# Optimization experiments

Measured on AMD Instinct MI355X. Metric: run time of the kernel, lower is better.

## Reference

```python
import jax, jax.numpy as jnp
import numpy as np

NUM_HEAD = 8
ATTN_DIM = 512
WINDOW_WIDTH = 31
HALF_WIN = WINDOW_WIDTH // 2  # symmetric band half-width
NEG_INF = -1e10


def setup_inputs() -> dict:
    key = jax.random.key(0)
    k0, k1, k2 = jax.random.split(key, 3)
    n, c, w = 4, 512, 2048
    out_dim = 512
    input_ = jax.random.normal(k0, (n, c, 1, w), dtype=jnp.float32)
    mask = jnp.ones((n, w), dtype=jnp.float32)  # 1 = valid key position
    # xavier-uniform-like init for the two linears, zero bias (as in the module)
    lim_in = np.sqrt(6.0 / (c + 3 * ATTN_DIM)).astype(np.float32)
    W_in = jax.random.uniform(k1, (3 * ATTN_DIM, c), jnp.float32, -lim_in, lim_in)
    b_in = jnp.zeros((3 * ATTN_DIM,), jnp.float32)
    lim_fc = np.sqrt(6.0 / (ATTN_DIM + out_dim)).astype(np.float32)
    W_fc = jax.random.uniform(k2, (out_dim, ATTN_DIM), jnp.float32, -lim_fc, lim_fc)
    b_fc = jnp.zeros((out_dim,), jnp.float32)
    return {"input_": input_, "mask": mask, "W_in": W_in, "b_in": b_in,
            "W_fc": W_fc, "b_fc": b_fc}


def reference(input_, mask, W_in, b_in, W_fc, b_fc):
    n, c, h, w = input_.shape  # h == 1
    d = ATTN_DIM // NUM_HEAD
    x = input_.reshape(n, c, w).transpose(0, 2, 1)          # [n, w, c]
    temp = x @ W_in.T + b_in                                # [n, w, 3A]
    temp = temp.transpose(0, 2, 1)                          # [n, 3A, w]
    # channel layout after chunk(num_head) then chunk(3): [h, {q,k,v}, d]
    qkv = temp.reshape(n, NUM_HEAD, 3, d, w)
    q, k, v = qkv[:, :, 0], qkv[:, :, 1], qkv[:, :, 2]      # each [n, H, d, w]
    scale = NUM_HEAD / ATTN_DIM                              # == 1/d_head
    attn = jnp.einsum('nhdi,nhdj->nhij', q, k) * scale       # [n, H, w, w]
    # windowed band mask combined with per-key padding mask (clip_mask/mha_mask)
    idx = jnp.arange(w)
    band = jnp.abs(idx[:, None] - idx[None, :]) <= HALF_WIN  # [w, w]
    valid = band[None, None, :, :] & (mask > 0.5)[:, None, None, :]
    attn = jnp.where(valid, attn, NEG_INF)                   # pre-softmax mask
    attn = jax.nn.softmax(attn, axis=-1)
    attn = jnp.where(valid, attn, 0.0)                       # post-softmax mask
    # dropout in eval mode (identity) for a deterministic reference
    out = jnp.einsum('nhdj,nhij->nhdi', v, attn)             # [n, H, d, w]
    out = out.reshape(n, ATTN_DIM, w).transpose(0, 2, 1)     # [n, w, A]
    out = out @ W_fc.T + b_fc                                # [n, w, out_dim]
    od = out.shape[-1]
    return out.transpose(0, 2, 1).reshape(n, od, 1, w)
```

## Files before the change

kernel.cpp:

```cpp
#include <hip/hip_runtime.h>
#include <hip/hip_bf16.h>
#include <math.h>

#define W_SEQ   2048
#define C_IN    512
#define N_BATCH 4
#define NHEAD   8
#define QKV_CH  1536
#define OUT_CH  512
#define ATTND   512
#define N1_4    (QKV_CH * C_IN / 4)
#define N2_4    (OUT_CH * ATTND / 4)

typedef __attribute__((ext_vector_type(8))) short bf16x8;
typedef __attribute__((ext_vector_type(8))) unsigned short u16x8;
typedef __attribute__((ext_vector_type(4))) float f32x4;

__device__ __forceinline__ void gld16(const void* g, void* l) {
    __builtin_amdgcn_global_load_lds((const __attribute__((address_space(1))) void*)g,
                                     (__attribute__((address_space(3))) void*)l, 16, 0, 0);
}
__device__ __forceinline__ unsigned short f2bf(float f) {
    unsigned u = __float_as_uint(f);
    return (unsigned short)((u + 0x7FFFu + ((u >> 16) & 1u)) >> 16);
}
__device__ __forceinline__ unsigned ld_flag(const unsigned* p) {
    return __hip_atomic_load(p, __ATOMIC_RELAXED, __HIP_MEMORY_SCOPE_AGENT);
}


__device__ __forceinline__ void prep_unit(char* sm, int b,
    const float* __restrict__ input, unsigned short* __restrict__ Xh,
    const float* __restrict__ W_in, unsigned short* __restrict__ Winh,
    const float* __restrict__ W_fc, unsigned short* __restrict__ Wfch)
{
    const int t = threadIdx.x;
    float (*ts)[65] = (float(*)[65])sm;
    const int n  = b >> 8, rm = b & 255;
    const int i0 = (rm & 31) * 64, c0 = (rm >> 5) * 64;
    const int tx = t & 63, ty = t >> 6;
    #pragma unroll
    for (int s = 0; s < 16; ++s) {
        const int c = s * 4 + ty;
        ts[c][tx] = input[((size_t)(n * C_IN + c0 + c)) * W_SEQ + i0 + tx];
    }
    __syncthreads();
    const int c8 = t & 7, il = t >> 3;
    #pragma unroll
    for (int s = 0; s < 2; ++s) {
        const int i = il + 32 * s;
        u16x8 hv;
        #pragma unroll
        for (int e = 0; e < 8; ++e) hv[e] = f2bf(ts[c8 * 8 + e][i]);
        *(u16x8*)(&Xh[((size_t)(n * W_SEQ + i0 + i)) * C_IN + c0 + c8 * 8]) = hv;
    }
    const int idx = b * 256 + t;
    if (idx < N1_4) {
        const float4 v = ((const float4*)W_in)[idx];
        ushort4 hh; hh.x = f2bf(v.x); hh.y = f2bf(v.y); hh.z = f2bf(v.z); hh.w = f2bf(v.w);
        ((ushort4*)Winh)[idx] = hh;
    } else {
        const int j = idx - N1_4;
        const float4 v = ((const float4*)W_fc)[j];
        ushort4 hh; hh.x = f2bf(v.x); hh.y = f2bf(v.y); hh.z = f2bf(v.z); hh.w = f2bf(v.w);
        ((ushort4*)Wfch)[j] = hh;
    }
}

template<int EPI>
__device__ __forceinline__ void gemm_body(char* sm, int bx, int by,
    const unsigned short* __restrict__ A, const unsigned short* __restrict__ B,
    const float* __restrict__ bias, void* __restrict__ Cv, const int ldc)
{
    const int t = threadIdx.x;
    const int l = t & 63, w = t >> 6;
    const int m0 = by * 128, n0 = bx * 128;
    const int wm = w >> 1, wn = w & 1;

    const int subrow = l >> 3;
    const int swz    = ((l & 7) ^ subrow) << 4;
    const char* pA = (const char*)A + (size_t)m0 * 1024 + swz;
    const char* pB = (const char*)B + (size_t)n0 * 1024 + swz;

    const int frow = l & 15;
    f32x4 acc[4][4] = {};

    for (int k0 = 0; k0 < 512; k0 += 64) {
        const int kb = k0 * 2;
        #pragma unroll
        for (int c = 0; c < 4; ++c) {
            const int q = 4 * w + c;
            const size_t roff = (size_t)(q * 8 + subrow) * 1024 + kb;
            gld16(pA + roff, sm +         q * 1024);
            gld16(pB + roff, sm + 16384 + q * 1024);
        }
        __syncthreads();
        #pragma unroll
        for (int kk = 0; kk < 2; ++kk) {
            const int cswz = (kk * 64 + ((l >> 4) << 4)) ^ ((l & 7) << 4);
            bf16x8 a[4], b[4];
            #pragma unroll
            for (int mi = 0; mi < 4; ++mi)
                a[mi] = *(const bf16x8*)(sm + (wm * 64 + mi * 16 + frow) * 128 + cswz);
            #pragma unroll
            for (int ni = 0; ni < 4; ++ni)
                b[ni] = *(const bf16x8*)(sm + 16384 + (wn * 64 + ni * 16 + frow) * 128 + cswz);
            #pragma unroll
            for (int mi = 0; mi < 4; ++mi)
                #pragma unroll
                for (int ni = 0; ni < 4; ++ni)
                    acc[mi][ni] = __builtin_amdgcn_mfma_f32_16x16x32_bf16(a[mi], b[ni], acc[mi][ni], 0, 0, 0);
        }
        __syncthreads();
    }

    const int g = l >> 4;
    int cols[4]; float bcol[4];
    #pragma unroll
    for (int ni = 0; ni < 4; ++ni) {
        cols[ni] = n0 + wn * 64 + ni * 16 + frow;
        bcol[ni] = (EPI == 0) ? bias[cols[ni]] : 0.f;
    }
    #pragma unroll
    for (int mi = 0; mi < 4; ++mi) {
        #pragma unroll
        for (int r = 0; r < 4; ++r) {
            const int rowg = m0 + wm * 64 + mi * 16 + g * 4 + r;
            float brow = 0.f;
            if (EPI == 1) brow = bias[rowg];
            #pragma unroll
            for (int ni = 0; ni < 4; ++ni) {
                const float v = acc[mi][ni][r];
                if (EPI == 0) {
                    ((unsigned short*)Cv)[(size_t)rowg * ldc + cols[ni]] = f2bf(v + bcol[ni]);
                } else {
                    const int nb = cols[ni] >> 11, ii = cols[ni] & (W_SEQ - 1);
                    ((float*)Cv)[((size_t)(nb * OUT_CH + rowg)) * W_SEQ + ii] = v + brow;
                }
            }
        }
    }
}

#define VT_OFF  13824
#define MSK_OFF 30208

__device__ __forceinline__ void attn_body(char* sm, int blk,
    const unsigned short* __restrict__ qkv, const float* __restrict__ mask,
    unsigned short* __restrict__ aoh)
{
    const int t = threadIdx.x, l = t & 63, w = t >> 6;
    const int i0 = (blk & 31) * 64, h = (blk >> 5) & 7, n = blk >> 8;
    const int lr = l & 15, lg = l >> 4;

    const char* tb = (const char*)qkv + ((size_t)n * W_SEQ * QKV_CH + h * 192) * 2;

    const int r8 = l >> 3, c8 = l & 7;
    #pragma unroll
    for (int it = 0; it < 3; ++it) {
        const int jl = w * 24 + it * 8 + r8;
        const int jg = i0 - 16 + jl;
        bf16x8 kv = {}, vv = {};
        if (jg >= 0 && jg < W_SEQ) {
            const char* rp = tb + (size_t)jg * 3072;
            kv = *(const bf16x8*)(rp + 128 + c8 * 16);
            vv = *(const bf16x8*)(rp + 256 + c8 * 16);
        }
        *(bf16x8*)(sm + jl * 144 + c8 * 16) = kv;
        const int J0 = jl >> 3;
        #pragma unroll
        for (int e = 0; e < 8; ++e) {
            const int d = c8 * 8 + e;
            const int fold = ((d >> 3) ^ d) & 7;
            *(unsigned short*)(sm + VT_OFF + d * 256 + (((J0 ^ fold) << 4) | ((jl & 7) * 2)))
                = (unsigned short)vv[e];
        }
    }
    bf16x8 qh[2];
    {
        const char* qrow = tb + (size_t)(i0 + w * 16 + lr) * 3072 + lg * 16;
        qh[0] = *(const bf16x8*)(qrow);
        qh[1] = *(const bf16x8*)(qrow + 64);
    }
    if (t < 96) {
        const int jg = i0 - 16 + t;
        *(float*)(sm + MSK_OFF + t * 4) = (jg >= 0 && jg < W_SEQ) ? mask[n * W_SEQ + jg] : 0.f;
    }
    __syncthreads();

    f32x4 sacc[6] = {};
    #pragma unroll
    for (int nf = 0; nf < 6; ++nf) {
        #pragma unroll
        for (int kk = 0; kk < 2; ++kk) {
            const bf16x8 kh = *(const bf16x8*)(sm + (nf * 16 + lr) * 144 + kk * 64 + lg * 16);
            sacc[nf] = __builtin_amdgcn_mfma_f32_16x16x32_bf16(qh[kk], kh, sacc[nf], 0, 0, 0);
        }
    }
    __syncthreads();

    float mv[6];
    #pragma unroll
    for (int nf = 0; nf < 6; ++nf)
        mv[nf] = *(const float*)(sm + MSK_OFF + (nf * 16 + lr) * 4);

    #pragma unroll
    for (int r = 0; r < 4; ++r) {
        const int ri = w * 16 + lg * 4 + r;
        float sv[6], mrow = -1.0e30f;
        #pragma unroll
        for (int nf = 0; nf < 6; ++nf) {
            const int jcol = nf * 16 + lr;
            const bool valid = (jcol > ri) && (jcol <= ri + 31) && (mv[nf] > 0.5f);
            const float s = valid ? sacc[nf][r] * 0.015625f : -1.0e30f;
            sv[nf] = s;
            mrow = fmaxf(mrow, s);
        }
        #pragma unroll
        for (int off = 1; off <= 8; off <<= 1) mrow = fmaxf(mrow, __shfl_xor(mrow, off));
        float ls = 0.f;
        #pragma unroll
        for (int nf = 0; nf < 6; ++nf) {
            float pp = __expf(sv[nf] - mrow);
            pp = (sv[nf] > -1.0e29f) ? pp : 0.f;
            sv[nf] = pp;
            ls += pp;
        }
        #pragma unroll
        for (int off = 1; off <= 8; off <<= 1) ls += __shfl_xor(ls, off);
        const float rinv = (ls > 0.f) ? 1.f / ls : 0.f;
        #pragma unroll
        for (int nf = 0; nf < 6; ++nf)
            *(unsigned short*)(sm + ri * 208 + (nf * 16 + lr) * 2) = f2bf(sv[nf] * rinv);
    }

    f32x4 oacc[4] = {};
    #pragma unroll
    for (int ks = 0; ks < 3; ++ks) {
        const bf16x8 pah = *(const bf16x8*)(sm + (w * 16 + lr) * 208 + ks * 64 + lg * 16);
        #pragma unroll
        for (int nf2 = 0; nf2 < 4; ++nf2) {
            const int dd = nf2 * 16 + lr;
            const int fold = ((dd >> 3) ^ dd) & 7;
            const bf16x8 vb = *(const bf16x8*)(sm + VT_OFF + dd * 256 + (((4 * ks + lg) ^ fold) << 4));
            oacc[nf2] = __builtin_amdgcn_mfma_f32_16x16x32_bf16(pah, vb, oacc[nf2], 0, 0, 0);
        }
    }

    #pragma unroll
    for (int nf2 = 0; nf2 < 4; ++nf2) {
        #pragma unroll
        for (int r = 0; r < 4; ++r) {
            const int ri = w * 16 + lg * 4 + r;
            aoh[((size_t)(n * W_SEQ + i0 + ri)) * ATTND + h * 64 + nf2 * 16 + lr] = f2bf(oacc[nf2][r]);
        }
    }
}

__global__ __launch_bounds__(256, 4) void fused_all_k(
    const float* __restrict__ input, const float* __restrict__ mask,
    const float* __restrict__ W_in,  const float* __restrict__ b_in,
    const float* __restrict__ W_fc,  const float* __restrict__ b_fc,
    float* __restrict__ out,
    unsigned short* __restrict__ QKVh, unsigned short* __restrict__ AOh,
    unsigned short* __restrict__ Winh, unsigned short* __restrict__ Wfch,
    unsigned short* __restrict__ Xh, unsigned* __restrict__ flg)
{
    __shared__ __align__(16) char sm[32768];
    const int b = blockIdx.x;
    unsigned* xdone  = flg;
    unsigned* wpanel = flg + 1024;
    unsigned* wfc    = flg + 1280;
    unsigned* qdone  = flg + 2048;
    unsigned* adone  = flg + 3072;

    prep_unit(sm, b, input, Xh, W_in, Winh, W_fc, Wfch);
    __syncthreads();
    if (threadIdx.x == 0) {
        __threadfence();
        atomicAdd(xdone + ((b >> 8) * 16 + ((b & 31) >> 1)) * 16, 1u);
        if (b < 768) atomicAdd(wpanel + (b >> 6) * 16, 1u);
        else         atomicAdd(wfc, 1u);
    }

    if (b < 768) {
        const int y8 = b & 7, r = b >> 3;
        const int bx = r % 12;
        const int by = (((r / 12) + 6) & 7) * 8 + y8;
        if (threadIdx.x == 0) {
            while (ld_flag(wpanel + bx * 16) < 64u) __builtin_amdgcn_s_sleep(2);
            while (ld_flag(xdone  + by * 16) < 16u) __builtin_amdgcn_s_sleep(2);
            __threadfence();
        }
        __syncthreads();
        gemm_body<0>(sm, bx, by, Xh, Winh, b_in, QKVh, QKV_CH);
        __syncthreads();
        if (threadIdx.x == 0) {
            __threadfence();
            atomicAdd(qdone + by * 16, 1u);
        }
    }

    {
        const int n = b >> 8, i0 = (b & 31) * 64;
        const int row1 = n * W_SEQ + ((i0 >= 16) ? i0 - 16 : 0);
        const int row2 = n * W_SEQ + ((i0 + 79 <= W_SEQ - 1) ? i0 + 79 : W_SEQ - 1);
        const int t1 = row1 >> 7, t2 = row2 >> 7;
        if (threadIdx.x == 0) {
            while (ld_flag(qdone + t1 * 16) < 12u) __builtin_amdgcn_s_sleep(2);
            while (ld_flag(qdone + t2 * 16) < 12u) __builtin_amdgcn_s_sleep(2);
            __threadfence();
        }
        __syncthreads();
        attn_body(sm, b, QKVh, mask, AOh);
        __syncthreads();
        if (threadIdx.x == 0) {
            __threadfence();
            const int panel = n * 16 + (i0 >> 7);
            atomicAdd(adone + panel * 16, 1u);
        }
    }

    if (b < 256) {
        const int bx = b >> 2, by = b & 3;
        if (threadIdx.x == 0) {
            while (ld_flag(wfc) < 256u) __builtin_amdgcn_s_sleep(2);
            while (ld_flag(adone + bx * 16) < 16u) __builtin_amdgcn_s_sleep(2);
            __threadfence();
        }
        __syncthreads();
        gemm_body<1>(sm, bx, by, Wfch, AOh, b_fc, out, 0);
    }
}

__global__ __launch_bounds__(256, 4) void prep_sep_k(
    const float* __restrict__ input, unsigned short* __restrict__ Xh,
    const float* __restrict__ W_in, unsigned short* __restrict__ Winh,
    const float* __restrict__ W_fc, unsigned short* __restrict__ Wfch)
{
    __shared__ __align__(16) char sm[32768];
    prep_unit(sm, blockIdx.x, input, Xh, W_in, Winh, W_fc, Wfch);
}
__global__ __launch_bounds__(256, 4) void gemm1_sep_k(
    const unsigned short* __restrict__ A, const unsigned short* __restrict__ B,
    const float* __restrict__ bias, unsigned short* __restrict__ C)
{
    __shared__ __align__(16) char sm[32768];
    const int d = blockIdx.x, y8 = d & 7, r = d >> 3;
    gemm_body<0>(sm, r % 12, (((r / 12) + 6) & 7) * 8 + y8, A, B, bias, C, QKV_CH);
}
__global__ __launch_bounds__(256, 4) void attn_sep_k(
    const unsigned short* __restrict__ qkv, const float* __restrict__ mask,
    unsigned short* __restrict__ aoh)
{
    __shared__ __align__(16) char sm[32768];
    attn_body(sm, blockIdx.x, qkv, mask, aoh);
}
__global__ __launch_bounds__(256, 4) void gemm2_sep_k(
    const unsigned short* __restrict__ A, const unsigned short* __restrict__ B,
    const float* __restrict__ bias, float* __restrict__ out)
{
    __shared__ __align__(16) char sm[32768];
    gemm_body<1>(sm, blockIdx.x >> 2, blockIdx.x & 3, A, B, bias, out, 0);
}

extern "C" void kernel_launch(void* const* d_in, const int* in_sizes, int n_in,
                              void* d_out, int out_size, void* d_ws, size_t ws_size,
                              hipStream_t stream)
{
    const float* input = (const float*)d_in[0];
    const float* mask  = (const float*)d_in[1];
    const float* W_in  = (const float*)d_in[2];
    const float* b_in  = (const float*)d_in[3];
    const float* W_fc  = (const float*)d_in[4];
    const float* b_fc  = (const float*)d_in[5];
    float* out = (float*)d_out;
    char* ws = (char*)d_ws;

    unsigned short* QKVh = (unsigned short*)ws;
    unsigned short* AOh  = (unsigned short*)(ws + 25165824);
    unsigned short* Winh = (unsigned short*)(ws + 33554432);
    unsigned short* Wfch = (unsigned short*)(ws + 35127296);
    unsigned short* Xh   = (unsigned short*)(ws + 35651584);
    unsigned*       flg  = (unsigned*)(ws + 46137344);

    int occ = 0;
    hipOccupancyMaxActiveBlocksPerMultiprocessor(&occ, fused_all_k, 256, 0);

    if (occ >= 4) {
        hipMemsetAsync(flg, 0, 16384, stream);
        fused_all_k<<<dim3(1024), 256, 0, stream>>>(
            input, mask, W_in, b_in, W_fc, b_fc, out,
            QKVh, AOh, Winh, Wfch, Xh, flg);
    } else {
        prep_sep_k <<<dim3(1024), 256, 0, stream>>>(input, Xh, W_in, Winh, W_fc, Wfch);
        gemm1_sep_k<<<dim3(768),  256, 0, stream>>>(Xh, Winh, b_in, QKVh);
        attn_sep_k <<<dim3(1024), 256, 0, stream>>>(QKVh, mask, AOh);
        gemm2_sep_k<<<dim3(256),  256, 0, stream>>>(Wfch, AOh, b_fc, out);
    }
}
```

Before: 50.60 us.

## Use 32x32 MFMA in GEMMs, drop softmax max-subtraction, add setprio around MFMAs

Measured after the change: 52.01 us. 2.8% more time.

```diff
diff --git a/kernel.cpp b/kernel.cpp
--- a/kernel.cpp
+++ b/kernel.cpp
@@ -12,9 +12,10 @@
 #define N1_4    (QKV_CH * C_IN / 4)
 #define N2_4    (OUT_CH * ATTND / 4)
 
-typedef __attribute__((ext_vector_type(8))) short bf16x8;
-typedef __attribute__((ext_vector_type(8))) unsigned short u16x8;
-typedef __attribute__((ext_vector_type(4))) float f32x4;
+typedef __attribute__((ext_vector_type(8)))  short bf16x8;
+typedef __attribute__((ext_vector_type(8)))  unsigned short u16x8;
+typedef __attribute__((ext_vector_type(4)))  float f32x4;
+typedef __attribute__((ext_vector_type(16))) float f32x16;
 
 __device__ __forceinline__ void gld16(const void* g, void* l) {
     __builtin_amdgcn_global_load_lds((const __attribute__((address_space(1))) void*)g,
@@ -82,8 +83,8 @@
     const char* pA = (const char*)A + (size_t)m0 * 1024 + swz;
     const char* pB = (const char*)B + (size_t)n0 * 1024 + swz;
 
-    const int frow = l & 15;
-    f32x4 acc[4][4] = {};
+    const int l31 = l & 31, lh = l >> 5;
+    f32x16 acc[2][2] = {};
 
     for (int k0 = 0; k0 < 512; k0 += 64) {
         const int kb = k0 * 2;
@@ -96,46 +97,39 @@
         }
         __syncthreads();
         #pragma unroll
-        for (int kk = 0; kk < 2; ++kk) {
-            const int cswz = (kk * 64 + ((l >> 4) << 4)) ^ ((l & 7) << 4);
-            bf16x8 a[4], b[4];
+        for (int ks = 0; ks < 4; ++ks) {
+            const int cswz = (ks * 32 + (lh << 4)) ^ ((l & 7) << 4);
+            bf16x8 a[2], b[2];
             #pragma unroll
-            for (int mi = 0; mi < 4; ++mi)
-                a[mi] = *(const bf16x8*)(sm + (wm * 64 + mi * 16 + frow) * 128 + cswz);
+            for (int mi = 0; mi < 2; ++mi)
+                a[mi] = *(const bf16x8*)(sm + (wm * 64 + mi * 32 + l31) * 128 + cswz);
             #pragma unroll
-            for (int ni = 0; ni < 4; ++ni)
-                b[ni] = *(const bf16x8*)(sm + 16384 + (wn * 64 + ni * 16 + frow) * 128 + cswz);
+            for (int ni = 0; ni < 2; ++ni)
+                b[ni] = *(const bf16x8*)(sm + 16384 + (wn * 64 + ni * 32 + l31) * 128 + cswz);
             #pragma unroll
-            for (int mi = 0; mi < 4; ++mi)
+            for (int mi = 0; mi < 2; ++mi)
                 #pragma unroll
-                for (int ni = 0; ni < 4; ++ni)
-                    acc[mi][ni] = __builtin_amdgcn_mfma_f32_16x16x32_bf16(a[mi], b[ni], acc[mi][ni], 0, 0, 0);
-        }
-        __syncthreads();
-    }
-
-    const int g = l >> 4;
-    int cols[4]; float bcol[4];
-    #pragma unroll
-    for (int ni = 0; ni < 4; ++ni) {
-        cols[ni] = n0 + wn * 64 + ni * 16 + frow;
-        bcol[ni] = (EPI == 0) ? bias[cols[ni]] : 0.f;
-    }
-    #pragma unroll
-    for (int mi = 0; mi < 4; ++mi) {
-        #pragma unroll
-        for (int r = 0; r < 4; ++r) {
-            const int rowg = m0 + wm * 64 + mi * 16 + g * 4 + r;
-            float brow = 0.f;
-            if (EPI == 1) brow = bias[rowg];
+                for (int ni = 0; ni < 2; ++ni)
+                    acc[mi][ni] = __builtin_amdgcn_mfma_f32_32x32x16_bf16(a[mi], b[ni], acc[mi][ni], 0, 0, 0);
+        }
+        __syncthreads();
+    }
+
+    #pragma unroll
+    for (int mi = 0; mi < 2; ++mi) {
+        #pragma unroll
+        for (int ni = 0; ni < 2; ++ni) {
+            const int colg = n0 + wn * 64 + ni * 32 + l31;
+            const float bcol = (EPI == 0) ? bias[colg] : 0.f;
             #pragma unroll
-            for (int ni = 0; ni < 4; ++ni) {
+            for (int r = 0; r < 16; ++r) {
+                const int rowg = m0 + wm * 64 + mi * 32 + (r & 3) + 8 * (r >> 2) + 4 * lh;
                 const float v = acc[mi][ni][r];
                 if (EPI == 0) {
-                    ((unsigned short*)Cv)[(size_t)rowg * ldc + cols[ni]] = f2bf(v + bcol[ni]);
+                    ((unsigned short*)Cv)[(size_t)rowg * ldc + colg] = f2bf(v + bcol);
                 } else {
-                    const int nb = cols[ni] >> 11, ii = cols[ni] & (W_SEQ - 1);
-                    ((float*)Cv)[((size_t)(nb * OUT_CH + rowg)) * W_SEQ + ii] = v + brow;
+                    const int nb = colg >> 11, ii = colg & (W_SEQ - 1);
+                    ((float*)Cv)[((size_t)(nb * OUT_CH + rowg)) * W_SEQ + ii] = v + bias[rowg];
                 }
             }
         }
@@ -189,6 +183,7 @@
     __syncthreads();
 
     f32x4 sacc[6] = {};
+    __builtin_amdgcn_s_setprio(1);
     #pragma unroll
     for (int nf = 0; nf < 6; ++nf) {
         #pragma unroll
@@ -197,6 +192,7 @@
             sacc[nf] = __builtin_amdgcn_mfma_f32_16x16x32_bf16(qh[kk], kh, sacc[nf], 0, 0, 0);
         }
     }
+    __builtin_amdgcn_s_setprio(0);
     __syncthreads();
 
     float mv[6];
@@ -207,24 +203,14 @@
     #pragma unroll
     for (int r = 0; r < 4; ++r) {
         const int ri = w * 16 + lg * 4 + r;
-        float sv[6], mrow = -1.0e30f;
+        float sv[6], ls = 0.f;
         #pragma unroll
         for (int nf = 0; nf < 6; ++nf) {
             const int jcol = nf * 16 + lr;
             const bool valid = (jcol > ri) && (jcol <= ri + 31) && (mv[nf] > 0.5f);
-            const float s = valid ? sacc[nf][r] * 0.015625f : -1.0e30f;
-            sv[nf] = s;
-            mrow = fmaxf(mrow, s);
-        }
-        #pragma unroll
-        for (int off = 1; off <= 8; off <<= 1) mrow = fmaxf(mrow, __shfl_xor(mrow, off));
-        float ls = 0.f;
-        #pragma unroll
-        for (int nf = 0; nf < 6; ++nf) {
-            float pp = __expf(sv[nf] - mrow);
-            pp = (sv[nf] > -1.0e29f) ? pp : 0.f;
-            sv[nf] = pp;
-            ls += pp;
+            const float p = valid ? __expf(sacc[nf][r] * 0.015625f) : 0.f;
+            sv[nf] = p;
+            ls += p;
         }
         #pragma unroll
         for (int off = 1; off <= 8; off <<= 1) ls += __shfl_xor(ls, off);
@@ -235,6 +221,7 @@
     }
 
     f32x4 oacc[4] = {};
+    __builtin_amdgcn_s_setprio(1);
     #pragma unroll
     for (int ks = 0; ks < 3; ++ks) {
         const bf16x8 pah = *(const bf16x8*)(sm + (w * 16 + lr) * 208 + ks * 64 + lg * 16);
@@ -246,6 +233,7 @@
             oacc[nf2] = __builtin_amdgcn_mfma_f32_16x16x32_bf16(pah, vb, oacc[nf2], 0, 0, 0);
         }
     }
+    __builtin_amdgcn_s_setprio(0);
 
     #pragma unroll
     for (int nf2 = 0; nf2 < 4; ++nf2) {
```
